# Optimization experiments

Hardware: AMD Instinct MI355X
Metric: run time of the kernel (lower is better)

## Reference

```python
import jax, jax.numpy as jnp
import numpy as np

N_NODES = 100000
N_EDGES = 3200000
N_FEAT = 128
HIDDEN = 16
N_CLASSES = 10
N_GRAPHS = 512


def setup_inputs() -> dict:
    key = jax.random.key(0)
    ks = jax.random.split(key, 12)
    x = jax.random.normal(ks[0], (N_NODES, N_FEAT), dtype=jnp.float32)
    edge_index = jax.random.randint(ks[1], (2, N_EDGES), 0, N_NODES, dtype=jnp.int64)
    batch = jnp.sort(jax.random.randint(ks[2], (N_NODES,), 0, N_GRAPHS, dtype=jnp.int64))
    def glorot(k, fan_in, fan_out):
        s = jnp.sqrt(6.0 / (fan_in + fan_out)).astype(jnp.float32)
        return jax.random.uniform(k, (fan_in, fan_out), jnp.float32, -s, s)
    W1 = glorot(ks[3], N_FEAT, HIDDEN); b1 = jnp.zeros((HIDDEN,), jnp.float32)
    W2 = glorot(ks[4], HIDDEN, HIDDEN); b2 = jnp.zeros((HIDDEN,), jnp.float32)
    W3 = glorot(ks[5], HIDDEN, HIDDEN); b3 = jnp.zeros((HIDDEN,), jnp.float32)
    Wlin = glorot(ks[6], HIDDEN, N_CLASSES)
    blin = jnp.zeros((N_CLASSES,), jnp.float32)
    return {"x": x, "edge_index": edge_index, "batch": batch,
            "W1": W1, "b1": b1, "W2": W2, "b2": b2, "W3": W3, "b3": b3,
            "Wlin": Wlin, "blin": blin}


def _gcn_conv(x, W, b, src, dst, norm, n):
    # h = X W ; out[dst] += norm * h[src] ; + bias
    h = x @ W
    out = jax.ops.segment_sum(h[src] * norm[:, None], dst, num_segments=n)
    return out + b


def reference(x, edge_index, batch, W1, b1, W2, b2, W3, b3, Wlin, blin):
    n = x.shape[0]
    loop = jnp.arange(n, dtype=edge_index.dtype)
    src = jnp.concatenate([edge_index[0], loop])  # add self-loops (PyG GCNConv default)
    dst = jnp.concatenate([edge_index[1], loop])
    # symmetric degree normalization: deg over destination (incl. self-loops)
    deg = jax.ops.segment_sum(jnp.ones_like(dst, dtype=x.dtype), dst, num_segments=n)
    dinv = jnp.where(deg > 0, jax.lax.rsqrt(jnp.maximum(deg, 1.0)), 0.0)
    norm = dinv[src] * dinv[dst]  # [E+N]

    h = jax.nn.relu(_gcn_conv(x, W1, b1, src, dst, norm, n))
    h = jax.nn.relu(_gcn_conv(h, W2, b2, src, dst, norm, n))
    h = _gcn_conv(h, W3, b3, src, dst, norm, n)
    # global add pool over graphs
    pooled = jax.ops.segment_sum(h, batch, num_segments=N_GRAPHS)  # [G, hidden]
    # dropout p=0.5 is identity in eval mode
    return pooled @ Wlin + blin
```

## Files before the change

kernel.cpp:

```cpp
#include <hip/hip_runtime.h>
#include <hip/hip_fp16.h>

#define N_NODES   100000
#define N_EDGES   3200000
#define N_FEAT    128
#define HIDDEN    16
#define N_CLASSES 10
#define N_GRAPHS  512
#define NPB       256
#define NBUCKET   391
#define EPB       4096
#define PBLK      ((N_EDGES + EPB - 1) / EPB)
#define PSLACK    15872
#define CSLACK    9216


__global__ void cursor_init_kernel(int* __restrict__ cur) {
    int i = blockIdx.x * 256 + threadIdx.x;
    if (i < NBUCKET) cur[i] = i * PSLACK;
}

__global__ __launch_bounds__(512) void partition_kernel(const int* __restrict__ src,
                                                        const int* __restrict__ dst,
                                                        int* __restrict__ cur,
                                                        unsigned* __restrict__ part) {
    __shared__ int cnt[NBUCKET];
    __shared__ int lbase[NBUCKET];
    __shared__ int rk[NBUCKET];
    __shared__ int gbase[NBUCKET];
    __shared__ int s[512];
    __shared__ unsigned sorted[EPB];
    __shared__ unsigned short bb[EPB];
    __shared__ unsigned char  dl[EPB];
    int tid = threadIdx.x;
    for (int i = tid; i < NBUCKET; i += 512) cnt[i] = 0;
    __syncthreads();
    int s0 = blockIdx.x * EPB;
#pragma unroll
    for (int i = 0; i < EPB / 512; ++i) {
        int le = i * 512 + tid;
        int e  = s0 + le;
        if (e < N_EDGES) {
            int d = dst[e];
            int b = d >> 8;
            bb[le] = (unsigned short)b;
            dl[le] = (unsigned char)(d & 255);
            atomicAdd(&cnt[b], 1);
        }
    }
    __syncthreads();
    int v = (tid < NBUCKET) ? cnt[tid] : 0;
    s[tid] = v;
    __syncthreads();
    for (int off = 1; off < 512; off <<= 1) {
        int t = (tid >= off) ? s[tid - off] : 0;
        __syncthreads();
        s[tid] += t;
        __syncthreads();
    }
    if (tid < NBUCKET) {
        int lb = s[tid] - v;
        lbase[tid] = lb;
        rk[tid]    = lb;
        int cpad = (v + 15) & ~15;
        gbase[tid] = cpad ? atomicAdd(&cur[tid], cpad) : 0;
    }
    __syncthreads();
#pragma unroll
    for (int i = 0; i < EPB / 512; ++i) {
        int le = i * 512 + tid;
        int e  = s0 + le;
        if (e < N_EDGES) {
            int b = bb[le];
            int r = atomicAdd(&rk[b], 1);
            sorted[r] = (unsigned)src[e] | ((unsigned)dl[le] << 17);
        }
    }
    __syncthreads();
    int w16 = tid >> 4, l16 = tid & 15;
    for (int b = w16; b < NBUCKET; b += 32) {
        int c = cnt[b];
        if (!c) continue;
        int cpad = (c + 15) & ~15;
        int lb = lbase[b], gb = gbase[b];
        for (int j = l16; j < cpad; j += 16)
            part[gb + j] = (j < c) ? sorted[lb + j] : 0xFFFFFFFFu;
    }
}

__global__ __launch_bounds__(512) void build_csr_kernel(const unsigned* __restrict__ part,
                                                        const int* __restrict__ cur,
                                                        int2* __restrict__ rp,
                                                        float* __restrict__ dinv, int* __restrict__ csr) {
    __shared__ int ncnt[256];
    __shared__ int s[512];
    int b   = blockIdx.x;
    int tid = threadIdx.x;
    int beg = b * PSLACK, end = cur[b];
    if (tid < 256) ncnt[tid] = 0;
    __syncthreads();
    for (int j = beg + tid; j < end; j += 512) {
        unsigned r = part[j];
        if (r != 0xFFFFFFFFu) atomicAdd(&ncnt[(r >> 17) & 255], 1);
    }
    __syncthreads();
    int deg = (tid < 256) ? ncnt[tid] : 0;
    s[tid] = deg;
    __syncthreads();
    for (int off = 1; off < 512; off <<= 1) {
        int t = (tid >= off) ? s[tid - off] : 0;
        __syncthreads();
        s[tid] += t;
        __syncthreads();
    }
    int excl = s[tid] - deg;
    int cbeg = b * CSLACK;
    if (tid < 256) {
        int node = b * 256 + tid;
        if (node < N_NODES) {
            rp[node]   = make_int2(cbeg + excl, cbeg + excl + deg);
            dinv[node] = rsqrtf((float)(deg + 1));
        }
    }
    __syncthreads();
    if (tid < 256) ncnt[tid] = cbeg + excl;
    __syncthreads();
    for (int j = beg + tid; j < end; j += 512) {
        unsigned r = part[j];
        if (r != 0xFFFFFFFFu) {
            int vv = (r >> 17) & 255;
            int slot = atomicAdd(&ncnt[vv], 1);
            csr[slot] = (int)(r & 0x1FFFFu);
        }
    }
}


__device__ __forceinline__ void pack_store8(__half* outp, int idx, const float* o) {
    int4 w;
    __half2 q;
    q = __floats2half2_rn(o[0], o[1]); w.x = *(int*)&q;
    q = __floats2half2_rn(o[2], o[3]); w.y = *(int*)&q;
    q = __floats2half2_rn(o[4], o[5]); w.z = *(int*)&q;
    q = __floats2half2_rn(o[6], o[7]); w.w = *(int*)&q;
    ((int4*)outp)[idx] = w;
}

__global__ __launch_bounds__(256) void transform_x_kernel(const float* __restrict__ x,
                                                          const float* __restrict__ W,
                                                          const float* __restrict__ dinv,
                                                          __half* __restrict__ g) {
    __shared__ __half2 Wp[1024];
    int tid = threadIdx.x;
    for (int i = tid; i < 1024; i += 256) {
        int kp = i >> 4, f = i & 15;
        Wp[i] = __floats2half2_rn(W[(2 * kp) * HIDDEN + f], W[(2 * kp + 1) * HIDDEN + f]);
    }
    __syncthreads();
    int l  = tid & 63;
    int wv = tid >> 6;
    int rw = l >> 2;
    int q  = l & 3;
    int row = blockIdx.x * 64 + wv * 16 + rw;
    if (row >= N_NODES) return;
    const float4* xp = (const float4*)x + (size_t)row * 32;
    float4 xr[8];
#pragma unroll
    for (int s8 = 0; s8 < 8; ++s8) xr[s8] = xp[q + 4 * s8];
    __half2 acc[16];
    const __half2 z2 = __floats2half2_rn(0.f, 0.f);
#pragma unroll
    for (int f = 0; f < 16; ++f) acc[f] = z2;
    const int4* w4 = (const int4*)Wp;
#pragma unroll
    for (int s8 = 0; s8 < 8; ++s8) {
        int k4 = q + 4 * s8;
        __half2 xp0 = __floats2half2_rn(xr[s8].x, xr[s8].y);
        __half2 xp1 = __floats2half2_rn(xr[s8].z, xr[s8].w);
#pragma unroll
        for (int hf = 0; hf < 2; ++hf) {
            int kp = 2 * k4 + hf;
            __half2 xv = hf ? xp1 : xp0;
#pragma unroll
            for (int j = 0; j < 4; ++j) {
                int4 wj = w4[kp * 4 + j];
                const __half2* wvv = (const __half2*)&wj;
#pragma unroll
                for (int ff = 0; ff < 4; ++ff)
                    acc[j * 4 + ff] = __hfma2(xv, wvv[ff], acc[j * 4 + ff]);
            }
        }
    }
    float di = dinv[row];
    float o[16];
#pragma unroll
    for (int f = 0; f < 16; ++f) {
        float2 t = __half22float2(acc[f]);
        float sv = t.x + t.y;
        sv += __shfl_xor(sv, 1);
        sv += __shfl_xor(sv, 2);
        o[f] = sv * di;
    }
    if (q == 0) {
        pack_store8(g, row * 2,     &o[0]);
        pack_store8(g, row * 2 + 1, &o[8]);
    }
}

template <int MODE>
__global__ __launch_bounds__(256) void aggregate_kernel(
        const __half* __restrict__ g, const int2* __restrict__ rp,
        const int* __restrict__ csr, const float* __restrict__ dinv,
        const float* __restrict__ bias, const float* __restrict__ Wn,
        __half* __restrict__ out) {
    __shared__ float WnL[HIDDEN * HIDDEN];
    int tid  = threadIdx.x;
    if (MODE == 2) {
        if (tid < HIDDEN * HIDDEN) WnL[tid] = Wn[tid];
        __syncthreads();
    }
    int wave = tid >> 6;
    int l    = tid & 63;
    int c  = l >> 3;
    int vl = (l >> 1) & 3;
    int hh = l & 1;
    int v = blockIdx.x * 16 + wave * 4 + vl;
    int2 range = rp[v];
    int beg = range.x, end = range.y;
    const int4* g4 = (const int4*)g;
    float a0 = 0.f, a1 = 0.f, a2 = 0.f, a3 = 0.f, a4 = 0.f, a5 = 0.f, a6 = 0.f, a7 = 0.f;
#pragma unroll 4
    for (int j = beg + c; j < end; j += 8) {
        int s = csr[j];
        int4 r = g4[s * 2 + hh];
        float2 f0 = __half22float2(*(const __half2*)&r.x);
        float2 f1 = __half22float2(*(const __half2*)&r.y);
        float2 f2 = __half22float2(*(const __half2*)&r.z);
        float2 f3 = __half22float2(*(const __half2*)&r.w);
        a0 += f0.x; a1 += f0.y; a2 += f1.x; a3 += f1.y;
        a4 += f2.x; a5 += f2.y; a6 += f3.x; a7 += f3.y;
    }
    a0 += __shfl_xor(a0, 8);  a1 += __shfl_xor(a1, 8);
    a2 += __shfl_xor(a2, 8);  a3 += __shfl_xor(a3, 8);
    a4 += __shfl_xor(a4, 8);  a5 += __shfl_xor(a5, 8);
    a6 += __shfl_xor(a6, 8);  a7 += __shfl_xor(a7, 8);
    a0 += __shfl_xor(a0, 16); a1 += __shfl_xor(a1, 16);
    a2 += __shfl_xor(a2, 16); a3 += __shfl_xor(a3, 16);
    a4 += __shfl_xor(a4, 16); a5 += __shfl_xor(a5, 16);
    a6 += __shfl_xor(a6, 16); a7 += __shfl_xor(a7, 16);
    a0 += __shfl_xor(a0, 32); a1 += __shfl_xor(a1, 32);
    a2 += __shfl_xor(a2, 32); a3 += __shfl_xor(a3, 32);
    a4 += __shfl_xor(a4, 32); a5 += __shfl_xor(a5, 32);
    a6 += __shfl_xor(a6, 32); a7 += __shfl_xor(a7, 32);
    if (c == 0) {
        int4 r = g4[v * 2 + hh];
        float2 s0 = __half22float2(*(const __half2*)&r.x);
        float2 s1 = __half22float2(*(const __half2*)&r.y);
        float2 s2 = __half22float2(*(const __half2*)&r.z);
        float2 s3 = __half22float2(*(const __half2*)&r.w);
        float di = dinv[v];
        const float4* bp = (const float4*)bias;
        float4 bA = bp[hh * 2];
        float4 bB = bp[hh * 2 + 1];
        float o[8];
        o[0] = di * (a0 + s0.x) + bA.x;
        o[1] = di * (a1 + s0.y) + bA.y;
        o[2] = di * (a2 + s1.x) + bA.z;
        o[3] = di * (a3 + s1.y) + bA.w;
        o[4] = di * (a4 + s2.x) + bB.x;
        o[5] = di * (a5 + s2.y) + bB.y;
        o[6] = di * (a6 + s3.x) + bB.z;
        o[7] = di * (a7 + s3.y) + bB.w;
        if (MODE == 2) {
#pragma unroll
            for (int i = 0; i < 8; ++i) o[i] = fmaxf(o[i], 0.f);
            float pa[16];
#pragma unroll
            for (int f = 0; f < 16; ++f) pa[f] = 0.f;
            const float* wr = &WnL[hh * 8 * HIDDEN];
#pragma unroll
            for (int qq = 0; qq < 8; ++qq) {
                float hq = o[qq];
#pragma unroll
                for (int f = 0; f < 16; ++f) pa[f] += hq * wr[qq * HIDDEN + f];
            }
            float o2[8];
#pragma unroll
            for (int i = 0; i < 8; ++i) {
                float lo = pa[i];
                float hi = pa[8 + i];
                float keep = hh ? hi : lo;
                float send = hh ? lo : hi;
                float recv = __shfl_xor(send, 1);
                o2[i] = di * (keep + recv);
            }
            pack_store8(out, v * 2 + hh, o2);
        } else {
            pack_store8(out, v * 2 + hh, o);
        }
    }
}


__global__ void pool_head_kernel(const __half* __restrict__ h, const int* __restrict__ batch,
                                 const float* __restrict__ Wlin, const float* __restrict__ blin,
                                 float* __restrict__ out) {
    __shared__ float red[256];
    __shared__ int bounds[2];
    int g   = blockIdx.x;
    int tid = threadIdx.x;
    if (tid < 2) {
        int target = g + tid;
        int lo = 0, hi = N_NODES;
        while (lo < hi) {
            int mid = (lo + hi) >> 1;
            if (batch[mid] < target) lo = mid + 1; else hi = mid;
        }
        bounds[tid] = lo;
    }
    __syncthreads();
    int start = bounds[0], end = bounds[1];
    int f = tid & 15, r = tid >> 4;
    float acc = 0.f;
    for (int v = start + r; v < end; v += 16)
        acc += __half2float(h[v * HIDDEN + f]);
    red[tid] = acc;
    __syncthreads();
    for (int off = 128; off >= 16; off >>= 1) {
        if (tid < off) red[tid] += red[tid + off];
        __syncthreads();
    }
    if (tid < N_CLASSES) {
        float s = blin[tid];
#pragma unroll
        for (int fe = 0; fe < HIDDEN; ++fe) s += red[fe] * Wlin[fe * N_CLASSES + tid];
        out[g * N_CLASSES + tid] = s;
    }
}


extern "C" void kernel_launch(void* const* d_in, const int* in_sizes, int n_in,
                              void* d_out, int out_size, void* d_ws, size_t ws_size,
                              hipStream_t stream) {
    const float* x     = (const float*)d_in[0];
    const int*   ei    = (const int*)d_in[1];
    const int*   src   = ei;
    const int*   dst   = ei + N_EDGES;
    const int*   batch = (const int*)d_in[2];
    const float* W1 = (const float*)d_in[3];
    const float* b1 = (const float*)d_in[4];
    const float* W2 = (const float*)d_in[5];
    const float* b2 = (const float*)d_in[6];
    const float* W3 = (const float*)d_in[7];
    const float* b3 = (const float*)d_in[8];
    const float* Wlin = (const float*)d_in[9];
    const float* blin = (const float*)d_in[10];
    float* out = (float*)d_out;

    char* w = (char*)d_ws;
    auto alloc = [&](size_t bytes) -> char* {
        char* p = w;
        w += (bytes + 255) & ~(size_t)255;
        return p;
    };
    int*    cur    = (int*)alloc((size_t)NBUCKET * 4);
    int2*   rp     = (int2*)alloc((size_t)N_NODES * 8);
    float*  dinv   = (float*)alloc((size_t)N_NODES * 4);
    __half* gA     = (__half*)alloc((size_t)N_NODES * HIDDEN * 2);
    __half* gB     = (__half*)alloc((size_t)N_NODES * HIDDEN * 2);
    __half* hA     = (__half*)alloc((size_t)N_NODES * HIDDEN * 2);
    unsigned* part = (unsigned*)alloc((size_t)NBUCKET * PSLACK * 4);
    int*    csr    = (int*)alloc((size_t)NBUCKET * CSLACK * 4);

    int ntx = (N_NODES + 63) / 64;
    int ab  = (N_NODES + 15) / 16;

    cursor_init_kernel<<<(NBUCKET + 255) / 256, 256, 0, stream>>>(cur);
    partition_kernel<<<PBLK, 512, 0, stream>>>(src, dst, cur, part);
    build_csr_kernel<<<NBUCKET, 512, 0, stream>>>(part, cur, rp, dinv, csr);

    transform_x_kernel<<<ntx, 256, 0, stream>>>(x, W1, dinv, gA);
    aggregate_kernel<2><<<ab, 256, 0, stream>>>(gA, rp, csr, dinv, b1, W2, gB);
    aggregate_kernel<2><<<ab, 256, 0, stream>>>(gB, rp, csr, dinv, b2, W3, gA);
    aggregate_kernel<0><<<ab, 256, 0, stream>>>(gA, rp, csr, dinv, b3, nullptr, hA);

    pool_head_kernel<<<N_GRAPHS, 256, 0, stream>>>(hA, batch, Wlin, blin, out);
}
```

Measured before the change: 263.7 us.

## Use nontemporal loads/stores, memset cursor init, and cache per-edge rank in CSR build

Switches streaming edge, partition, x and CSR reads/writes to nontemporal builtins so single-use data goes around the caches. The cursor-init kernel is replaced by a hipMemsetAsync, with bucket offsets now added in partition and build. build_csr keeps each edge's local rank in shared memory, so the second pass needs no atomics. The aggregate kernel issues its row-pointer load before the weight-staging barrier. Nontemporal hints on csr, which is reread across three layers, could cost cache hits, and the extra 15.9KB of shared memory lowers occupancy in build_csr.

```diff
diff --git a/kernel.cpp b/kernel.cpp
--- a/kernel.cpp
+++ b/kernel.cpp
@@ -14,11 +14,8 @@
 #define PSLACK    15872
 #define CSLACK    9216
 
-
-__global__ void cursor_init_kernel(int* __restrict__ cur) {
-    int i = blockIdx.x * 256 + threadIdx.x;
-    if (i < NBUCKET) cur[i] = i * PSLACK;
-}
+typedef float vf4 __attribute__((ext_vector_type(4)));
+
 
 __global__ __launch_bounds__(512) void partition_kernel(const int* __restrict__ src,
                                                         const int* __restrict__ dst,
@@ -41,7 +38,7 @@
         int le = i * 512 + tid;
         int e  = s0 + le;
         if (e < N_EDGES) {
-            int d = dst[e];
+            int d = __builtin_nontemporal_load(&dst[e]);
             int b = d >> 8;
             bb[le] = (unsigned short)b;
             dl[le] = (unsigned char)(d & 255);
@@ -63,7 +60,7 @@
         lbase[tid] = lb;
         rk[tid]    = lb;
         int cpad = (v + 15) & ~15;
-        gbase[tid] = cpad ? atomicAdd(&cur[tid], cpad) : 0;
+        gbase[tid] = tid * PSLACK + (cpad ? atomicAdd(&cur[tid], cpad) : 0);
     }
     __syncthreads();
 #pragma unroll
@@ -73,7 +70,7 @@
         if (e < N_EDGES) {
             int b = bb[le];
             int r = atomicAdd(&rk[b], 1);
-            sorted[r] = (unsigned)src[e] | ((unsigned)dl[le] << 17);
+            sorted[r] = (unsigned)__builtin_nontemporal_load(&src[e]) | ((unsigned)dl[le] << 17);
         }
     }
     __syncthreads();
@@ -84,7 +81,7 @@
         int cpad = (c + 15) & ~15;
         int lb = lbase[b], gb = gbase[b];
         for (int j = l16; j < cpad; j += 16)
-            part[gb + j] = (j < c) ? sorted[lb + j] : 0xFFFFFFFFu;
+            __builtin_nontemporal_store((j < c) ? sorted[lb + j] : 0xFFFFFFFFu, &part[gb + j]);
     }
 }
 
@@ -94,14 +91,16 @@
                                                         float* __restrict__ dinv, int* __restrict__ csr) {
     __shared__ int ncnt[256];
     __shared__ int s[512];
+    __shared__ unsigned char rkb[PSLACK];
     int b   = blockIdx.x;
     int tid = threadIdx.x;
-    int beg = b * PSLACK, end = cur[b];
+    int beg = b * PSLACK, end = beg + cur[b];
     if (tid < 256) ncnt[tid] = 0;
     __syncthreads();
     for (int j = beg + tid; j < end; j += 512) {
-        unsigned r = part[j];
-        if (r != 0xFFFFFFFFu) atomicAdd(&ncnt[(r >> 17) & 255], 1);
+        unsigned r = __builtin_nontemporal_load(&part[j]);
+        if (r != 0xFFFFFFFFu)
+            rkb[j - beg] = (unsigned char)atomicAdd(&ncnt[(r >> 17) & 255], 1);
     }
     __syncthreads();
     int deg = (tid < 256) ? ncnt[tid] : 0;
@@ -126,12 +125,9 @@
     if (tid < 256) ncnt[tid] = cbeg + excl;
     __syncthreads();
     for (int j = beg + tid; j < end; j += 512) {
-        unsigned r = part[j];
-        if (r != 0xFFFFFFFFu) {
-            int vv = (r >> 17) & 255;
-            int slot = atomicAdd(&ncnt[vv], 1);
-            csr[slot] = (int)(r & 0x1FFFFu);
-        }
+        unsigned r = __builtin_nontemporal_load(&part[j]);
+        if (r != 0xFFFFFFFFu)
+            csr[ncnt[(r >> 17) & 255] + rkb[j - beg]] = (int)(r & 0x1FFFFu);
     }
 }
 
@@ -163,10 +159,10 @@
     int q  = l & 3;
     int row = blockIdx.x * 64 + wv * 16 + rw;
     if (row >= N_NODES) return;
-    const float4* xp = (const float4*)x + (size_t)row * 32;
-    float4 xr[8];
-#pragma unroll
-    for (int s8 = 0; s8 < 8; ++s8) xr[s8] = xp[q + 4 * s8];
+    const vf4* xp = (const vf4*)(x + (size_t)row * N_FEAT);
+    vf4 xr[8];
+#pragma unroll
+    for (int s8 = 0; s8 < 8; ++s8) xr[s8] = __builtin_nontemporal_load(&xp[q + 4 * s8]);
     __half2 acc[16];
     const __half2 z2 = __floats2half2_rn(0.f, 0.f);
 #pragma unroll
@@ -215,10 +211,6 @@
         __half* __restrict__ out) {
     __shared__ float WnL[HIDDEN * HIDDEN];
     int tid  = threadIdx.x;
-    if (MODE == 2) {
-        if (tid < HIDDEN * HIDDEN) WnL[tid] = Wn[tid];
-        __syncthreads();
-    }
     int wave = tid >> 6;
     int l    = tid & 63;
     int c  = l >> 3;
@@ -226,12 +218,16 @@
     int hh = l & 1;
     int v = blockIdx.x * 16 + wave * 4 + vl;
     int2 range = rp[v];
+    if (MODE == 2) {
+        if (tid < HIDDEN * HIDDEN) WnL[tid] = Wn[tid];
+        __syncthreads();
+    }
     int beg = range.x, end = range.y;
     const int4* g4 = (const int4*)g;
     float a0 = 0.f, a1 = 0.f, a2 = 0.f, a3 = 0.f, a4 = 0.f, a5 = 0.f, a6 = 0.f, a7 = 0.f;
 #pragma unroll 4
     for (int j = beg + c; j < end; j += 8) {
-        int s = csr[j];
+        int s = __builtin_nontemporal_load(&csr[j]);
         int4 r = g4[s * 2 + hh];
         float2 f0 = __half22float2(*(const __half2*)&r.x);
         float2 f1 = __half22float2(*(const __half2*)&r.y);
@@ -375,7 +371,7 @@
     int ntx = (N_NODES + 63) / 64;
     int ab  = (N_NODES + 15) / 16;
 
-    cursor_init_kernel<<<(NBUCKET + 255) / 256, 256, 0, stream>>>(cur);
+    (void)hipMemsetAsync(cur, 0, (size_t)NBUCKET * 4, stream);
     partition_kernel<<<PBLK, 512, 0, stream>>>(src, dst, cur, part);
     build_csr_kernel<<<NBUCKET, 512, 0, stream>>>(part, cur, rp, dinv, csr);
 
```

Result: slower. 303.7 us (+15.1%).
